# Optimization experiments

Hardware: AMD Instinct MI355X
Metric: run time of the kernel (lower is better)

Reference implementation:

```python
import jax, jax.numpy as jnp
import numpy as np

N = 50000        # nodes
E = 400000       # edges per relation graph
IN_DIM = 64
HID = 128
OUT_DIM = 2
NSEL = 4096
EPS = 0.3        # residual scale
SLOPE = 0.3      # LeakyReLU negative slope


def _leaky(x):
    return jnp.where(x >= 0, x, SLOPE * x)


def _deg_norm(dst):
    # FAGCN-style d = in_degree^{-1/2}; 0 for isolated nodes
    deg = jax.ops.segment_sum(jnp.ones(dst.shape[0], jnp.float32), dst, num_segments=N)
    return jnp.where(deg > 0, jax.lax.rsqrt(jnp.maximum(deg, 1.0)), 0.0)


def _gnn_layer(hf, src, dst, d, gw, gb):
    # gate(concat[h_dst, h_src]) computed as per-node projections then edge gather
    D = hf.shape[1]
    s_dst = hf @ gw[:D]   # [N]
    s_src = hf @ gw[D:]   # [N]
    a = jnp.tanh(s_dst[dst] + s_src[src] + gb)        # [E]
    e = a * d[dst] * d[src]                            # [E]
    msg = hf[src] * e[:, None]                         # [E, D]
    return jax.ops.segment_sum(msg, dst, num_segments=N)


def setup_inputs() -> dict:
    key = jax.random.key(0)
    ks = iter(jax.random.split(key, 48))
    def nrm(shape, scale=0.05):
        return jax.random.normal(next(ks), shape, jnp.float32) * scale
    inp = {}
    inp["h"] = jax.random.normal(next(ks), (N, IN_DIM), jnp.float32)
    for i in (1, 2, 3):
        inp[f"src{i}"] = jax.random.randint(next(ks), (E,), 0, N)
        inp[f"dst{i}"] = jax.random.randint(next(ks), (E,), 0, N)
    inp["nodes"] = jax.random.randint(next(ks), (NSEL,), 0, N)
    inp["t1_w"] = nrm((HID, IN_DIM)); inp["t1_b"] = jnp.zeros((HID,), jnp.float32)
    for i in (1, 2, 3):
        inp[f"gate1_{i}_w"] = nrm((2 * HID,)); inp[f"gate1_{i}_b"] = jnp.zeros((), jnp.float32)
        inp[f"gate2_{i}_w"] = nrm((6 * HID,)); inp[f"gate2_{i}_b"] = jnp.zeros((), jnp.float32)
        inp[f"hw1_{i}"] = nrm((HID, HID))
        inp[f"hw2_{i}"] = nrm((3 * HID, HID))
    inp["t2_w"] = nrm((64, 7 * HID + IN_DIM)); inp["t2_b"] = jnp.zeros((64,), jnp.float32)
    inp["t3_w"] = nrm((OUT_DIM, 64)); inp["t3_b"] = jnp.zeros((OUT_DIM,), jnp.float32)
    return inp


def reference(h, src1, dst1, src2, dst2, src3, dst3, nodes,
              t1_w, t1_b,
              gate1_1_w, gate1_1_b, gate1_2_w, gate1_2_b, gate1_3_w, gate1_3_b,
              gate2_1_w, gate2_1_b, gate2_2_w, gate2_2_b, gate2_3_w, gate2_3_b,
              hw1_1, hw1_2, hw1_3, hw2_1, hw2_2, hw2_3,
              t2_w, t2_b, t3_w, t3_b):
    d1, d2, d3 = _deg_norm(dst1), _deg_norm(dst2), _deg_norm(dst3)
    raw0 = h
    raw1 = _leaky(h @ t1_w.T + t1_b)   # [N, HID] (dropout=identity in eval)
    h1_1 = _leaky((EPS * raw1 + _gnn_layer(raw1, src1, dst1, d1, gate1_1_w, gate1_1_b)) @ hw1_1)
    h1_2 = _leaky((EPS * raw1 + _gnn_layer(raw1, src2, dst2, d2, gate1_2_w, gate1_2_b)) @ hw1_2)
    h1_3 = _leaky((EPS * raw1 + _gnn_layer(raw1, src3, dst3, d3, gate1_3_w, gate1_3_b)) @ hw1_3)
    raw2 = jnp.concatenate([h1_1, h1_2, h1_3], axis=1)   # [N, 3*HID]
    h2_1 = _leaky((EPS * raw2 + _gnn_layer(raw2, src1, dst1, d1, gate2_1_w, gate2_1_b)) @ hw2_1)
    h2_2 = _leaky((EPS * raw2 + _gnn_layer(raw2, src2, dst2, d2, gate2_2_w, gate2_2_b)) @ hw2_2)
    h2_3 = _leaky((EPS * raw2 + _gnn_layer(raw2, src3, dst3, d3, gate2_3_w, gate2_3_b)) @ hw2_3)
    hf = jnp.concatenate([h2_1, h2_2, h2_3, raw0, raw1, raw2], axis=1)  # [N, 7*HID+IN_DIM]
    nf = hf[nodes]                                       # [NSEL, 7*HID+IN_DIM]
    s = _leaky(nf @ t2_w.T + t2_b)
    return s @ t3_w.T + t3_b                             # [NSEL, OUT_DIM]
```

## Files before the change

kernel.cpp:

```cpp
#include <hip/hip_runtime.h>
#include <hip/hip_bf16.h>

#define NN 50000
#define NE 400000
#define IND 64
#define HID 128
#define H3 384
#define FDIM 960
#define NSEL 4096
#define EPSF 0.3f
#define SLOPEF 0.3f
#define SCHUNK 2048
#define NCHUNK 25
#define NBK 196
#define BCAP 4096
#define EPB 4096
#define NOEDGE 0xFFFFFFFFu

typedef __attribute__((ext_vector_type(8))) short bfrag;
typedef __attribute__((ext_vector_type(4))) float f4;
typedef __attribute__((ext_vector_type(8))) unsigned short us8;

__device__ __forceinline__ float leaky1(float v){ return v>=0.f? v : SLOPEF*v; }
__device__ __forceinline__ float b2f(unsigned short u){
  return __uint_as_float(((unsigned)u)<<16);
}
__device__ __forceinline__ unsigned short f2b(float v){
  __hip_bfloat16 b = __float2bfloat16(v);
  return *(unsigned short*)&b;
}

__global__ __launch_bounds__(256) void k_bfill4(
    const int* __restrict__ s0,const int* __restrict__ d0,
    const int* __restrict__ s1,const int* __restrict__ d1,
    const int* __restrict__ s2,const int* __restrict__ d2,
    int* __restrict__ bcnt, unsigned int* __restrict__ pairbuf)
{
  __shared__ unsigned int lbuf[EPB];
  __shared__ int hist[256];
  __shared__ int lbase[256];
  __shared__ int lcur[256];
  __shared__ int gbase[NBK];
  __shared__ int wsum[4];
  const int r = blockIdx.y;
  const int* S = (r==0)?s0:((r==1)?s1:s2);
  const int* D = (r==0)?d0:((r==1)?d1:d2);
  const int e0 = blockIdx.x*EPB;
  const int t = threadIdx.x;
  hist[t] = 0; lcur[t] = 0;
  __syncthreads();

  unsigned int pv[16];
  #pragma unroll
  for (int j=0;j<4;j++){
    int e = e0 + (j*256 + t)*4;
    if (e < NE){
      int4 sv = *(const int4*)&S[e];
      int4 dv = *(const int4*)&D[e];
      pv[j*4+0] = ((unsigned)dv.x<<16)|(unsigned)sv.x;
      pv[j*4+1] = ((unsigned)dv.y<<16)|(unsigned)sv.y;
      pv[j*4+2] = ((unsigned)dv.z<<16)|(unsigned)sv.z;
      pv[j*4+3] = ((unsigned)dv.w<<16)|(unsigned)sv.w;
    } else {
      pv[j*4+0]=NOEDGE; pv[j*4+1]=NOEDGE; pv[j*4+2]=NOEDGE; pv[j*4+3]=NOEDGE;
    }
  }
  #pragma unroll
  for (int i=0;i<16;i++){
    if (pv[i] != NOEDGE){
      atomicAdd(&hist[pv[i]>>24], 1);
    }
  }
  __syncthreads();
  {
    int hv = hist[t];
    int lane = t & 63, wid = t >> 6;
    int x = hv;
    #pragma unroll
    for (int d=1; d<64; d<<=1){ int y=__shfl_up(x,(unsigned)d); if(lane>=d) x+=y; }
    if (lane==63) wsum[wid]=x;
    __syncthreads();
    int wpre = 0;
    if (wid>0) wpre += wsum[0];
    if (wid>1) wpre += wsum[1];
    if (wid>2) wpre += wsum[2];
    lbase[t] = wpre + x - hv;
    if (t < NBK){
      int hh = hist[t];
      gbase[t] = (hh>0) ? atomicAdd(&bcnt[r*NBK+t], hh) : 0;
    }
  }
  __syncthreads();
  #pragma unroll
  for (int i=0;i<16;i++){
    if (pv[i] != NOEDGE){
      int b = (int)(pv[i] >> 24);
      int pos = lbase[b] + atomicAdd(&lcur[b], 1);
      lbuf[pos] = pv[i];
    }
  }
  __syncthreads();
  int tot = min(NE - e0, EPB);
  for (int idx = t; idx < tot; idx += 256){
    unsigned int v = lbuf[idx];
    int b = (int)(v >> 24);
    pairbuf[((size_t)(r*NBK + b))*BCAP + gbase[b] + (idx - lbase[b])] = v;
  }
}

__global__ __launch_bounds__(256) void k_count(const unsigned int* __restrict__ pairbuf,
                                               const int* __restrict__ bcnt,
                                               int* __restrict__ deg){
  __shared__ int hist[256];
  int r = blockIdx.y, b = blockIdx.x;
  int nb0 = b << 8;
  int t = threadIdx.x;
  hist[t] = 0;
  __syncthreads();
  int cnt = bcnt[r*NBK + b];
  const unsigned int* pb = pairbuf + ((size_t)(r*NBK + b))*BCAP;
  for (int e = t; e < cnt; e += 256){
    atomicAdd(&hist[(int)(pb[e] >> 16) - nb0], 1);
  }
  __syncthreads();
  int nidx = nb0 + t;
  if (nidx < NN) deg[r*NN + nidx] = hist[t];
}

__global__ __launch_bounds__(256) void k_scan_a(const int* __restrict__ deg,
    int* __restrict__ off, int* __restrict__ bsum, float* __restrict__ dnv){
  int b = blockIdx.x;
  int r = b / NCHUNK, c = b - r*NCHUNK;
  const int* dg = deg + r*NN;
  int* o = off + r*(NN+1);
  int t = threadIdx.x;
  int base = c*SCHUNK + t*8;
  int v[8];
  #pragma unroll
  for (int j=0;j<8;j++){
    int i = base+j;
    int g = (i<NN)? dg[i] : 0;
    v[j] = g;
    if (i<NN) dnv[r*NN+i] = (g>0)? rsqrtf((float)g) : 0.f;
  }
  int s=0;
  #pragma unroll
  for (int j=0;j<8;j++){ s += v[j]; v[j] = s; }
  int lane = t & 63, wid = t >> 6;
  int x = s;
  #pragma unroll
  for (int d=1; d<64; d<<=1){ int y=__shfl_up(x,(unsigned)d); if(lane>=d) x+=y; }
  __shared__ int ws[4];
  if (lane==63) ws[wid]=x;
  __syncthreads();
  int wpre = 0;
  if (wid>0) wpre += ws[0];
  if (wid>1) wpre += ws[1];
  if (wid>2) wpre += ws[2];
  int excl = wpre + x - s;
  #pragma unroll
  for (int j=0;j<8;j++){ int i=base+j; if (i<NN) o[i+1] = excl + v[j]; }
  if (t==255) bsum[b] = wpre + x;
}

__global__ void k_scan_b(int* __restrict__ bsum){
  int r = threadIdx.x;
  if (r < 3){
    int run = 0;
    for (int c=0;c<NCHUNK;c++){
      int t = bsum[r*NCHUNK+c];
      bsum[r*NCHUNK+c] = run;
      run += t;
    }
  }
}

__global__ __launch_bounds__(256) void k_scan_c(int* __restrict__ off,
                                                const int* __restrict__ bsum){
  int b = blockIdx.x;
  int r = b / NCHUNK, c = b - r*NCHUNK;
  int add = bsum[b];
  int* o = off + r*(NN+1);
  if (threadIdx.x==0 && c==0) o[0]=0;
  int base = c*SCHUNK;
  for (int j=threadIdx.x; j<SCHUNK; j+=256){
    int i = base+j;
    if (i<NN) o[i+1] += add;
  }
}

__global__ __launch_bounds__(256) void k_bsort3(const unsigned int* __restrict__ pairbuf,
                                                const int* __restrict__ bcnt,
                                                const int* __restrict__ off,
                                                unsigned short* __restrict__ csrc){
  __shared__ unsigned short lout[BCAP];
  __shared__ int cur2[256];
  __shared__ int nbase[256];
  int r = blockIdx.y, b = blockIdx.x;
  int nb0 = b << 8;
  const int* offr = off + r*(NN+1);
  int t = threadIdx.x;
  cur2[t] = 0;
  int e0g = offr[nb0];
  int nidx = nb0 + t;
  nbase[t] = (nidx < NN) ? (offr[nidx] - e0g) : 0;
  __syncthreads();
  int cnt = bcnt[r*NBK + b];
  const unsigned int* pb = pairbuf + ((size_t)(r*NBK + b))*BCAP;
  for (int e = t; e < cnt; e += 256){
    unsigned int pv = pb[e];
    int p = (int)(pv >> 16) - nb0;
    int slot = atomicAdd(&cur2[p], 1);
    lout[nbase[p] + slot] = (unsigned short)(pv & 0xffffu);
  }
  __syncthreads();
  unsigned short* op = csrc + (size_t)r*NE + e0g;
  for (int idx = t; idx < cnt; idx += 256) op[idx] = lout[idx];
}

__global__ void k_wprep2(const float* __restrict__ t1w,
    const float* __restrict__ hw1_0, const float* __restrict__ hw1_1, const float* __restrict__ hw1_2,
    const float* __restrict__ hw2_0, const float* __restrict__ hw2_1, const float* __restrict__ hw2_2,
    const float* __restrict__ t2w, const float* __restrict__ h,
    unsigned short* __restrict__ wt1, unsigned short* __restrict__ w1t,
    unsigned short* __restrict__ w2t, unsigned short* __restrict__ wt2,
    unsigned short* __restrict__ hb){
  int t = blockIdx.x*256 + threadIdx.x;
  if (t < 8192){
    wt1[t] = f2b(t1w[t]);
  } else if (t < 57344){
    int e = t - 8192;
    int r = e / 16384, q = e - r*16384;
    int n = q >> 7, k = q & 127;
    const float* W = (r==0)?hw1_0:((r==1)?hw1_1:hw1_2);
    w1t[e] = f2b(W[k*HID + n]);
  } else if (t < 204800){
    int e = t - 57344;
    int r = e / 49152, q = e - r*49152;
    int n = q / H3, k = q - n*H3;
    const float* W = (r==0)?hw2_0:((r==1)?hw2_1:hw2_2);
    w2t[e] = f2b(W[k*HID + n]);
  } else if (t < 266240){
    int e = t - 204800;
    wt2[e] = f2b(t2w[e]);
  } else if (t < 666240){
    int q = t - 266240;
    const float4 a = ((const float4*)h)[q*2];
    const float4 b = ((const float4*)h)[q*2+1];
    us8 o;
    o[0]=f2b(a.x); o[1]=f2b(a.y); o[2]=f2b(a.z); o[3]=f2b(a.w);
    o[4]=f2b(b.x); o[5]=f2b(b.y); o[6]=f2b(b.z); o[7]=f2b(b.w);
    *(us8*)&hb[q*8] = o;
  }
}

__global__ __launch_bounds__(256) void k_mfma_t1(
    const unsigned short* __restrict__ Ab, const unsigned short* __restrict__ W,
    const float* __restrict__ bias, unsigned short* __restrict__ Cb)
{
  __shared__ short As[64][72];
  __shared__ short Bs[128][72];
  const int tid = threadIdx.x;
  const int bm = blockIdx.x*64;

  for (int q = tid; q < 64*8; q += 256){
    int row = q >> 3, c8 = q & 7;
    int grow = bm + row; grow = (grow < NN) ? grow : (NN-1);
    *(us8*)&As[row][c8*8] = *(const us8*)&Ab[(size_t)grow*IND + c8*8];
  }
  for (int q = tid; q < 128*8; q += 256){
    int n = q >> 3, c8 = q & 7;
    *(us8*)&Bs[n][c8*8] = *(const us8*)&W[n*IND + c8*8];
  }
  __syncthreads();

  const int wid = tid >> 6, lane = tid & 63;
  const int wrow = (wid & 1)*32, wcol = (wid >> 1)*64;
  const int fr = lane & 15, fq = lane >> 4;
  f4 acc[2][4];
  #pragma unroll
  for (int mi=0;mi<2;mi++)
    #pragma unroll
    for (int ni=0;ni<4;ni++) acc[mi][ni] = (f4){0.f,0.f,0.f,0.f};

  #pragma unroll
  for (int ks=0; ks<2; ks++){
    int kb = ks*32 + fq*8;
    bfrag a[2], b[4];
    #pragma unroll
    for (int mi=0;mi<2;mi++) a[mi] = *(const bfrag*)&As[wrow + mi*16 + fr][kb];
    #pragma unroll
    for (int ni=0;ni<4;ni++) b[ni] = *(const bfrag*)&Bs[wcol + ni*16 + fr][kb];
    #pragma unroll
    for (int mi=0;mi<2;mi++)
      #pragma unroll
      for (int ni=0;ni<4;ni++)
        acc[mi][ni] = __builtin_amdgcn_mfma_f32_16x16x32_bf16(a[mi], b[ni], acc[mi][ni], 0, 0, 0);
  }

  #pragma unroll
  for (int mi=0;mi<2;mi++){
    int row0 = bm + wrow + mi*16 + fq*4;
    #pragma unroll
    for (int j=0;j<4;j++){
      int row = row0 + j;
      if (row < NN){
        #pragma unroll
        for (int ni=0;ni<4;ni++){
          int col = wcol + ni*16 + fr;
          Cb[(size_t)row*HID + col] = f2b(leaky1(acc[mi][ni][j] + bias[col]));
        }
      }
    }
  }
}

__global__ __launch_bounds__(256) void k_mfma128(
    const unsigned short* __restrict__ Abf, const unsigned short* __restrict__ Wt,
    unsigned short* __restrict__ Cb, int M)
{
  __shared__ short As[64][136];
  __shared__ short Bs[128][136];
  const int r = blockIdx.y;
  const unsigned short* Ar = Abf + (size_t)r*M*HID;
  const unsigned short* W  = Wt + (size_t)r*HID*HID;
  const int tid = threadIdx.x;
  const int bm = blockIdx.x*64;

  for (int q = tid; q < 64*16; q += 256){
    int row = q >> 4, c8 = q & 15;
    int grow = bm + row; grow = (grow < M) ? grow : (M-1);
    *(us8*)&As[row][c8*8] = *(const us8*)&Ar[(size_t)grow*HID + c8*8];
  }
  for (int q = tid; q < 128*16; q += 256){
    int n = q >> 4, c8 = q & 15;
    *(us8*)&Bs[n][c8*8] = *(const us8*)&W[n*HID + c8*8];
  }
  __syncthreads();

  const int wid = tid >> 6, lane = tid & 63;
  const int wrow = (wid & 1)*32, wcol = (wid >> 1)*64;
  const int fr = lane & 15, fq = lane >> 4;
  f4 acc[2][4];
  #pragma unroll
  for (int mi=0;mi<2;mi++)
    #pragma unroll
    for (int ni=0;ni<4;ni++) acc[mi][ni] = (f4){0.f,0.f,0.f,0.f};

  #pragma unroll
  for (int ks=0; ks<4; ks++){
    int kb = ks*32 + fq*8;
    bfrag a[2], b[4];
    #pragma unroll
    for (int mi=0;mi<2;mi++) a[mi] = *(const bfrag*)&As[wrow + mi*16 + fr][kb];
    #pragma unroll
    for (int ni=0;ni<4;ni++) b[ni] = *(const bfrag*)&Bs[wcol + ni*16 + fr][kb];
    #pragma unroll
    for (int mi=0;mi<2;mi++)
      #pragma unroll
      for (int ni=0;ni<4;ni++)
        acc[mi][ni] = __builtin_amdgcn_mfma_f32_16x16x32_bf16(a[mi], b[ni], acc[mi][ni], 0, 0, 0);
  }

  const int coff = r*HID;
  #pragma unroll
  for (int mi=0;mi<2;mi++){
    int row0 = bm + wrow + mi*16 + fq*4;
    #pragma unroll
    for (int j=0;j<4;j++){
      int row = row0 + j;
      if (row < M){
        #pragma unroll
        for (int ni=0;ni<4;ni++){
          Cb[(size_t)row*H3 + coff + wcol + ni*16 + fr] = f2b(leaky1(acc[mi][ni][j]));
        }
      }
    }
  }
}

__global__ __launch_bounds__(256) void k_mfma384(
    const unsigned short* __restrict__ Abf, const unsigned short* __restrict__ Wt,
    unsigned short* __restrict__ nfb)
{
  __shared__ short As[32][72];
  __shared__ short Bs[128][72];
  const int r = blockIdx.y;
  const unsigned short* Ar = Abf + (size_t)r*NSEL*H3;
  const unsigned short* W  = Wt + (size_t)r*HID*H3;
  const int tid = threadIdx.x;
  const int bm = blockIdx.x*32;
  const int wid = tid >> 6, lane = tid & 63;
  const int fr = lane & 15, fq = lane >> 4;
  f4 acc[2][2];
  #pragma unroll
  for (int mi=0;mi<2;mi++)
    #pragma unroll
    for (int ni=0;ni<2;ni++) acc[mi][ni] = (f4){0.f,0.f,0.f,0.f};

  for (int kc=0; kc<6; kc++){
    for (int q = tid; q < 32*8; q += 256){
      int row = q >> 3, c8 = q & 7;
      *(us8*)&As[row][c8*8] = *(const us8*)&Ar[(size_t)(bm+row)*H3 + kc*64 + c8*8];
    }
    for (int q = tid; q < 128*8; q += 256){
      int n = q >> 3, c8 = q & 7;
      *(us8*)&Bs[n][c8*8] = *(const us8*)&W[(size_t)n*H3 + kc*64 + c8*8];
    }
    __syncthreads();
    #pragma unroll
    for (int ks=0; ks<2; ks++){
      int kb = ks*32 + fq*8;
      bfrag a[2], b[2];
      #pragma unroll
      for (int mi=0;mi<2;mi++) a[mi] = *(const bfrag*)&As[mi*16 + fr][kb];
      #pragma unroll
      for (int ni=0;ni<2;ni++) b[ni] = *(const bfrag*)&Bs[wid*32 + ni*16 + fr][kb];
      #pragma unroll
      for (int mi=0;mi<2;mi++)
        #pragma unroll
        for (int ni=0;ni<2;ni++)
          acc[mi][ni] = __builtin_amdgcn_mfma_f32_16x16x32_bf16(a[mi], b[ni], acc[mi][ni], 0, 0, 0);
    }
    __syncthreads();
  }

  #pragma unroll
  for (int mi=0;mi<2;mi++){
    int row0 = bm + mi*16 + fq*4;
    #pragma unroll
    for (int j=0;j<4;j++){
      int i = row0 + j;
      #pragma unroll
      for (int ni=0;ni<2;ni++){
        int col = wid*32 + ni*16 + fr;
        nfb[(size_t)i*FDIM + r*HID + col] = f2b(leaky1(acc[mi][ni][j]));
      }
    }
  }
}

__global__ __launch_bounds__(256) void k_mfma_t2(
    const unsigned short* __restrict__ Abf, const unsigned short* __restrict__ W,
    float* __restrict__ sbuf)
{
  __shared__ short As[32][72];
  __shared__ short Bs[64][72];
  const int tid = threadIdx.x;
  const int bm = blockIdx.x*32;
  const int wid = tid >> 6, lane = tid & 63;
  const int fr = lane & 15, fq = lane >> 4;
  f4 acc[2];
  acc[0] = (f4){0.f,0.f,0.f,0.f};
  acc[1] = (f4){0.f,0.f,0.f,0.f};

  for (int kc=0; kc<15; kc++){
    for (int q = tid; q < 32*8; q += 256){
      int row = q >> 3, c8 = q & 7;
      *(us8*)&As[row][c8*8] = *(const us8*)&Abf[(size_t)(bm+row)*FDIM + kc*64 + c8*8];
    }
    for (int q = tid; q < 64*8; q += 256){
      int n = q >> 3, c8 = q & 7;
      *(us8*)&Bs[n][c8*8] = *(const us8*)&W[(size_t)n*FDIM + kc*64 + c8*8];
    }
    __syncthreads();
    #pragma unroll
    for (int ks=0; ks<2; ks++){
      int kb = ks*32 + fq*8;
      bfrag a[2], b;
      a[0] = *(const bfrag*)&As[fr][kb];
      a[1] = *(const bfrag*)&As[16 + fr][kb];
      b = *(const bfrag*)&Bs[wid*16 + fr][kb];
      acc[0] = __builtin_amdgcn_mfma_f32_16x16x32_bf16(a[0], b, acc[0], 0, 0, 0);
      acc[1] = __builtin_amdgcn_mfma_f32_16x16x32_bf16(a[1], b, acc[1], 0, 0, 0);
    }
    __syncthreads();
  }

  #pragma unroll
  for (int mi=0;mi<2;mi++){
    int row0 = bm + mi*16 + fq*4;
    #pragma unroll
    for (int j=0;j<4;j++){
      sbuf[(size_t)(row0+j)*64 + wid*16 + fr] = acc[mi][j];
    }
  }
}

__global__ __launch_bounds__(256) void k_final_wave(
    const float* __restrict__ sbuf, const float* __restrict__ t2b,
    const float* __restrict__ t3w, const float* __restrict__ t3b,
    float* __restrict__ outp)
{
  int w = (blockIdx.x*256 + threadIdx.x) >> 6;
  int j = threadIdx.x & 63;
  if (w >= NSEL) return;
  float v = leaky1(sbuf[(size_t)w*64 + j] + t2b[j]);
  float a0 = v*t3w[j], a1 = v*t3w[64+j];
  #pragma unroll
  for (int sft=32;sft>0;sft>>=1){
    a0 += __shfl_down(a0,(unsigned)sft);
    a1 += __shfl_down(a1,(unsigned)sft);
  }
  if (j==0){
    outp[2*w+0] = a0 + t3b[0];
    outp[2*w+1] = a1 + t3b[1];
  }
}

template<int D>
__global__ __launch_bounds__(256) void k_scores_g(const unsigned short* __restrict__ X,
    const float* __restrict__ g0, const float* __restrict__ g1, const float* __restrict__ g2,
    float* __restrict__ sd, float* __restrict__ ss){
  const int tid = threadIdx.x;
  const int p = tid & 15;
  const int n = blockIdx.x*16 + (tid >> 4);
  const unsigned short* x = X + (size_t)n*D;
  float a0=0,a1=0,a2=0,a3=0,a4=0,a5=0;
  #pragma unroll
  for (int it=0; it<D/128; it++){
    int k = it*128 + p*8;
    us8 u = *(const us8*)&x[k];
    #pragma unroll
    for (int e=0;e<8;e++){
      float v = b2f(u[e]);
      a0 = fmaf(v, g0[k+e],   a0);  a1 = fmaf(v, g0[D+k+e], a1);
      a2 = fmaf(v, g1[k+e],   a2);  a3 = fmaf(v, g1[D+k+e], a3);
      a4 = fmaf(v, g2[k+e],   a4);  a5 = fmaf(v, g2[D+k+e], a5);
    }
  }
  #pragma unroll
  for (int s=8;s>0;s>>=1){
    a0 += __shfl_xor(a0,(unsigned)s); a1 += __shfl_xor(a1,(unsigned)s);
    a2 += __shfl_xor(a2,(unsigned)s); a3 += __shfl_xor(a3,(unsigned)s);
    a4 += __shfl_xor(a4,(unsigned)s); a5 += __shfl_xor(a5,(unsigned)s);
  }
  if (p==0){
    sd[0*NN+n]=a0; ss[0*NN+n]=a1;
    sd[1*NN+n]=a2; ss[1*NN+n]=a3;
    sd[2*NN+n]=a4; ss[2*NN+n]=a5;
  }
}

__global__ __launch_bounds__(256) void k_gather_f3z(
    const unsigned short* __restrict__ Xb,
    const int* __restrict__ off, const unsigned short* __restrict__ csrc,
    const float* __restrict__ sd, const float* __restrict__ ss,
    const float* __restrict__ dnv,
    const float* __restrict__ gb0, const float* __restrict__ gb1, const float* __restrict__ gb2,
    unsigned short* __restrict__ outp){
  const int tid = threadIdx.x;
  const int lane = tid & 63;
  const int wg = lane >> 4;
  const int p  = lane & 15;
  const int n = blockIdx.x*16 + (tid >> 4);
  us8 rv = *(const us8*)&Xb[(size_t)n*HID + p*8];
  float resid[8];
  #pragma unroll
  for (int i=0;i<8;i++) resid[i] = EPSF * b2f(rv[i]);

  for (int r=0;r<3;r++){
    const int* offr = off + r*(NN+1);
    const unsigned short* csr = csrc + (size_t)r*NE;
    const float* ssr = ss + r*NN;
    const float* dnr = dnv + r*NN;
    float gbv = ((r==0)?gb0:((r==1)?gb1:gb2))[0];
    float sd_n = sd[r*NN + n], dn_n = dnr[n];
    float acc[8];
    #pragma unroll
    for (int i=0;i<8;i++) acc[i] = resid[i];
    int p0 = offr[n], p1 = offr[n+1];
    for (int pc=p0; pc<p1; pc+=16){
      int m = min(16, p1-pc);
      int s = 0; float c = 0.f;
      if (p < m){
        s = csr[pc+p];
        c = tanhf(sd_n + ssr[s] + gbv) * dn_n * dnr[s];
      }
      for (int j=0;j<m;j++){
        int   sj = __shfl(s, wg*16+j);
        float cj = __shfl(c, wg*16+j);
        us8 v = *(const us8*)&Xb[(size_t)sj*HID + p*8];
        #pragma unroll
        for (int i=0;i<8;i++) acc[i] = fmaf(cj, b2f(v[i]), acc[i]);
      }
    }
    us8 o;
    #pragma unroll
    for (int i=0;i<8;i++) o[i] = f2b(acc[i]);
    *(us8*)&outp[((size_t)r*NN + n)*HID + p*8] = o;
  }
}

__global__ __launch_bounds__(256) void k_gather_sel3w2(const unsigned short* __restrict__ Xb,
    const int* __restrict__ nodes,
    const int* __restrict__ off, const unsigned short* __restrict__ csrc,
    const float* __restrict__ sd, const float* __restrict__ ss,
    const float* __restrict__ dnv,
    const float* __restrict__ gb0, const float* __restrict__ gb1, const float* __restrict__ gb2,
    unsigned short* __restrict__ outp){
  const int tid = threadIdx.x;
  const int lane = tid & 63;
  const int wg = lane >> 4;
  const int p  = lane & 15;
  const int i = blockIdx.x*16 + (tid >> 4);
  const int r = blockIdx.y;
  const int n = nodes[i];
  const int* offr = off + r*(NN+1);
  const unsigned short* csr = csrc + (size_t)r*NE;
  const float* ssr = ss + r*NN;
  const float* dnr = dnv + r*NN;
  float gbv = ((r==0)?gb0:((r==1)?gb1:gb2))[0];
  float sd_n = sd[r*NN + n], dn_n = dnr[n];
  float acc[3][8];
  #pragma unroll
  for (int cc=0;cc<3;cc++)
    #pragma unroll
    for (int q=0;q<8;q++) acc[cc][q]=0.f;
  int p0 = offr[n], p1 = offr[n+1];
  for (int pc=p0; pc<p1; pc+=16){
    int m = min(16, p1-pc);
    int s = 0; float c = 0.f;
    if (p < m){
      s = csr[pc+p];
      c = tanhf(sd_n + ssr[s] + gbv) * dn_n * dnr[s];
    }
    for (int j=0;j<m;j++){
      int   sj = __shfl(s, wg*16+j);
      float cj = __shfl(c, wg*16+j);
      const unsigned short* row = &Xb[(size_t)sj*H3];
      #pragma unroll
      for (int cc=0;cc<3;cc++){
        us8 v = *(const us8*)&row[cc*HID + p*8];
        #pragma unroll
        for (int q=0;q<8;q++) acc[cc][q] = fmaf(cj, b2f(v[q]), acc[cc][q]);
      }
    }
  }
  const unsigned short* xrow = &Xb[(size_t)n*H3];
  unsigned short* orow = &outp[((size_t)r*NSEL + i)*H3];
  #pragma unroll
  for (int cc=0;cc<3;cc++){
    us8 v = *(const us8*)&xrow[cc*HID + p*8];
    us8 o;
    #pragma unroll
    for (int q=0;q<8;q++) o[q] = f2b(fmaf(EPSF, b2f(v[q]), acc[cc][q]));
    *(us8*)&orow[cc*HID + p*8] = o;
  }
}

__global__ __launch_bounds__(256) void k_nf_fillb(const unsigned short* __restrict__ hb,
    const unsigned short* __restrict__ raw1b, const unsigned short* __restrict__ raw2b,
    const int* __restrict__ nodes, unsigned short* __restrict__ nfb){
  int t = blockIdx.x*256 + threadIdx.x;
  if (t >= NSEL*72) return;
  int i = t/72, c = t - i*72;
  int n = nodes[i];
  us8 v; int col;
  if (c < 8)       { v = *(const us8*)&hb[(size_t)n*IND + c*8];           col = 384 + c*8; }
  else if (c < 24) { int q=c-8;  v = *(const us8*)&raw1b[(size_t)n*HID + q*8]; col = 448 + q*8; }
  else             { int q=c-24; v = *(const us8*)&raw2b[(size_t)n*H3  + q*8]; col = 576 + q*8; }
  *(us8*)&nfb[(size_t)i*FDIM + col] = v;
}

extern "C" void kernel_launch(void* const* d_in, const int* in_sizes, int n_in,
                              void* d_out, int out_size, void* d_ws, size_t ws_size,
                              hipStream_t stream){
  if (n_in < 32) return;
  const float* h = (const float*)d_in[0];
  const int* src[3] = {(const int*)d_in[1], (const int*)d_in[3], (const int*)d_in[5]};
  const int* dst[3] = {(const int*)d_in[2], (const int*)d_in[4], (const int*)d_in[6]};
  const int* nodes = (const int*)d_in[7];
  const float* t1w = (const float*)d_in[8];
  const float* t1b = (const float*)d_in[9];

  bool dictOrder = (in_sizes[12] == 768);
  const float *g1w[3],*g1b[3],*g2w[3],*g2b[3],*hw1[3],*hw2[3];
  for (int r=0;r<3;r++){
    if (dictOrder){
      int base = 10 + r*6;
      g1w[r]=(const float*)d_in[base+0]; g1b[r]=(const float*)d_in[base+1];
      g2w[r]=(const float*)d_in[base+2]; g2b[r]=(const float*)d_in[base+3];
      hw1[r]=(const float*)d_in[base+4]; hw2[r]=(const float*)d_in[base+5];
    } else {
      g1w[r]=(const float*)d_in[10+2*r]; g1b[r]=(const float*)d_in[11+2*r];
      g2w[r]=(const float*)d_in[16+2*r]; g2b[r]=(const float*)d_in[17+2*r];
      hw1[r]=(const float*)d_in[22+r];   hw2[r]=(const float*)d_in[25+r];
    }
  }
  const float* t2w = (const float*)d_in[28];
  const float* t2b = (const float*)d_in[29];
  const float* t3w = (const float*)d_in[30];
  const float* t3b = (const float*)d_in[31];
  float* outp = (float*)d_out;

  char* w = (char*)d_ws;
  auto carve = [&](size_t bytes)->void*{
    void* p = (void*)w;
    w += ((bytes + 255) & ~size_t(255));
    return p;
  };
  int*   deg  = (int*)  carve((size_t)(3*NN+1024)*4);
  int*   bcnt = deg + 3*NN;
  int*   off  = (int*)  carve((size_t)3*(NN+1)*4);
  float* dnv  = (float*)carve((size_t)3*NN*4);
  int*   bsum = (int*)  carve((size_t)128*4);
  unsigned short* csrc = (unsigned short*)carve((size_t)3*NE*2);
  float* sd1  = (float*)carve((size_t)3*NN*4);
  float* ss1  = (float*)carve((size_t)3*NN*4);
  float* sd2  = (float*)carve((size_t)3*NN*4);
  float* ss2  = (float*)carve((size_t)3*NN*4);
  unsigned short* wt1 = (unsigned short*)carve((size_t)HID*IND*2);
  unsigned short* w1t = (unsigned short*)carve((size_t)3*HID*HID*2);
  unsigned short* w2t = (unsigned short*)carve((size_t)3*HID*H3*2);
  unsigned short* wt2 = (unsigned short*)carve((size_t)64*FDIM*2);
  unsigned short* hb  = (unsigned short*)carve((size_t)NN*IND*2);
  unsigned short* raw1b = (unsigned short*)carve((size_t)NN*HID*2);
  unsigned short* raw2b = (unsigned short*)carve((size_t)NN*H3*2);
  size_t ubytes = (size_t)3*NN*HID*2;
  float* ureg = (float*)carve(ubytes);
  unsigned int* pairbuf = (unsigned int*)ureg;
  unsigned short* pre1b = (unsigned short*)ureg;
  unsigned short* pre2b = (unsigned short*)ureg;
  float* sbuf = (float*)((char*)ureg + (size_t)16*1024*1024);
  unsigned short* nfb = (unsigned short*)carve((size_t)NSEL*FDIM*2);

  hipMemsetAsync(bcnt, 0, (size_t)1024*4, stream);
  k_bfill4<<<dim3((NE+EPB-1)/EPB, 3), 256, 0, stream>>>(
      src[0],dst[0],src[1],dst[1],src[2],dst[2], bcnt, pairbuf);
  k_count <<<dim3(NBK,3), 256, 0, stream>>>(pairbuf, bcnt, deg);
  k_scan_a<<<3*NCHUNK, 256, 0, stream>>>(deg, off, bsum, dnv);
  k_scan_b<<<1, 64, 0, stream>>>(bsum);
  k_scan_c<<<3*NCHUNK, 256, 0, stream>>>(off, bsum);
  k_bsort3<<<dim3(NBK,3), 256, 0, stream>>>(pairbuf, bcnt, off, csrc);

  k_wprep2<<<(666240+255)/256, 256, 0, stream>>>(
      t1w, hw1[0], hw1[1], hw1[2], hw2[0], hw2[1], hw2[2], t2w, h,
      wt1, w1t, w2t, wt2, hb);

  k_mfma_t1<<<(NN+63)/64, 256, 0, stream>>>(hb, wt1, t1b, raw1b);

  k_scores_g<HID><<<NN/16, 256, 0, stream>>>(raw1b, g1w[0], g1w[1], g1w[2], sd1, ss1);

  k_gather_f3z<<<NN/16, 256, 0, stream>>>(raw1b, off, csrc,
      sd1, ss1, dnv, g1b[0], g1b[1], g1b[2], pre1b);
  k_mfma128<<<dim3((NN+63)/64, 3), 256, 0, stream>>>(pre1b, w1t, raw2b, NN);

  k_scores_g<H3><<<NN/16, 256, 0, stream>>>(raw2b, g2w[0], g2w[1], g2w[2], sd2, ss2);

  k_gather_sel3w2<<<dim3(NSEL/16, 3), 256, 0, stream>>>(raw2b, nodes, off, csrc,
      sd2, ss2, dnv, g2b[0], g2b[1], g2b[2], pre2b);

  k_mfma384<<<dim3(NSEL/32, 3), 256, 0, stream>>>(pre2b, w2t, nfb);

  k_nf_fillb<<<(NSEL*72+255)/256, 256, 0, stream>>>(hb, raw1b, raw2b, nodes, nfb);

  k_mfma_t2<<<NSEL/32, 256, 0, stream>>>(nfb, wt2, sbuf);
  k_final_wave<<<(NSEL*64+255)/256, 256, 0, stream>>>(sbuf, t2b, t3w, t3b, outp);
}
```

Baseline: 207.3 us.

## Fuse CSR count/scan/sort into one bucket kernel and prefetch gather rows

Replaces the count, three-stage scan and bucket-sort kernels with a single kernel per bucket. Each block derives its global edge offset by reducing the preceding bucket counts, builds a local histogram and scan, and writes offsets, degree norms and sorted sources in one pass. This removes four launches and the degree array round-trip. The gather kernels also load row offsets up front and software-pipeline the neighbour row loads one edge ahead, hiding load latency at the cost of extra registers.

```diff
diff --git a/kernel.cpp b/kernel.cpp
--- a/kernel.cpp
+++ b/kernel.cpp
@@ -10,8 +10,6 @@
 #define NSEL 4096
 #define EPSF 0.3f
 #define SLOPEF 0.3f
-#define SCHUNK 2048
-#define NCHUNK 25
 #define NBK 196
 #define BCAP 4096
 #define EPB 4096
@@ -67,9 +65,7 @@
   }
   #pragma unroll
   for (int i=0;i<16;i++){
-    if (pv[i] != NOEDGE){
-      atomicAdd(&hist[pv[i]>>24], 1);
-    }
+    if (pv[i] != NOEDGE) atomicAdd(&hist[pv[i]>>24], 1);
   }
   __syncthreads();
   {
@@ -108,113 +104,72 @@
   }
 }
 
-__global__ __launch_bounds__(256) void k_count(const unsigned int* __restrict__ pairbuf,
-                                               const int* __restrict__ bcnt,
-                                               int* __restrict__ deg){
+__global__ __launch_bounds__(256) void k_bsort4(
+    const unsigned int* __restrict__ pairbuf,
+    const int* __restrict__ bcnt,
+    int* __restrict__ off, float* __restrict__ dnv,
+    unsigned short* __restrict__ csrc)
+{
+  __shared__ unsigned short lout[BCAP];
   __shared__ int hist[256];
-  int r = blockIdx.y, b = blockIdx.x;
-  int nb0 = b << 8;
-  int t = threadIdx.x;
-  hist[t] = 0;
-  __syncthreads();
-  int cnt = bcnt[r*NBK + b];
+  __shared__ int excl[256];
+  __shared__ int cur[256];
+  __shared__ int red[256];
+  __shared__ int wsum[4];
+  const int r = blockIdx.y, b = blockIdx.x;
+  const int nb0 = b << 8;
+  const int t = threadIdx.x;
+  red[t] = (t < b) ? bcnt[r*NBK + t] : 0;
+  hist[t] = 0; cur[t] = 0;
+  __syncthreads();
+  #pragma unroll
+  for (int sdv=128; sdv>0; sdv>>=1){
+    if (t < sdv) red[t] += red[t+sdv];
+    __syncthreads();
+  }
+  const int bbase = red[0];
+  const int cnt = bcnt[r*NBK + b];
   const unsigned int* pb = pairbuf + ((size_t)(r*NBK + b))*BCAP;
-  for (int e = t; e < cnt; e += 256){
-    atomicAdd(&hist[(int)(pb[e] >> 16) - nb0], 1);
+  unsigned int pv[16];
+  #pragma unroll
+  for (int j=0;j<16;j++){
+    int e = j*256 + t;
+    pv[j] = (e < cnt) ? pb[e] : NOEDGE;
+    if (pv[j] != NOEDGE) atomicAdd(&hist[(int)(pv[j]>>16) - nb0], 1);
+  }
+  __syncthreads();
+  {
+    int hv = hist[t];
+    int lane = t & 63, wid = t >> 6;
+    int x = hv;
+    #pragma unroll
+    for (int d=1; d<64; d<<=1){ int y=__shfl_up(x,(unsigned)d); if(lane>=d) x+=y; }
+    if (lane==63) wsum[wid]=x;
+    __syncthreads();
+    int wpre = 0;
+    if (wid>0) wpre += wsum[0];
+    if (wid>1) wpre += wsum[1];
+    if (wid>2) wpre += wsum[2];
+    excl[t] = wpre + x - hv;
   }
   __syncthreads();
   int nidx = nb0 + t;
-  if (nidx < NN) deg[r*NN + nidx] = hist[t];
-}
-
-__global__ __launch_bounds__(256) void k_scan_a(const int* __restrict__ deg,
-    int* __restrict__ off, int* __restrict__ bsum, float* __restrict__ dnv){
-  int b = blockIdx.x;
-  int r = b / NCHUNK, c = b - r*NCHUNK;
-  const int* dg = deg + r*NN;
-  int* o = off + r*(NN+1);
-  int t = threadIdx.x;
-  int base = c*SCHUNK + t*8;
-  int v[8];
-  #pragma unroll
-  for (int j=0;j<8;j++){
-    int i = base+j;
-    int g = (i<NN)? dg[i] : 0;
-    v[j] = g;
-    if (i<NN) dnv[r*NN+i] = (g>0)? rsqrtf((float)g) : 0.f;
-  }
-  int s=0;
-  #pragma unroll
-  for (int j=0;j<8;j++){ s += v[j]; v[j] = s; }
-  int lane = t & 63, wid = t >> 6;
-  int x = s;
-  #pragma unroll
-  for (int d=1; d<64; d<<=1){ int y=__shfl_up(x,(unsigned)d); if(lane>=d) x+=y; }
-  __shared__ int ws[4];
-  if (lane==63) ws[wid]=x;
-  __syncthreads();
-  int wpre = 0;
-  if (wid>0) wpre += ws[0];
-  if (wid>1) wpre += ws[1];
-  if (wid>2) wpre += ws[2];
-  int excl = wpre + x - s;
-  #pragma unroll
-  for (int j=0;j<8;j++){ int i=base+j; if (i<NN) o[i+1] = excl + v[j]; }
-  if (t==255) bsum[b] = wpre + x;
-}
-
-__global__ void k_scan_b(int* __restrict__ bsum){
-  int r = threadIdx.x;
-  if (r < 3){
-    int run = 0;
-    for (int c=0;c<NCHUNK;c++){
-      int t = bsum[r*NCHUNK+c];
-      bsum[r*NCHUNK+c] = run;
-      run += t;
-    }
-  }
-}
-
-__global__ __launch_bounds__(256) void k_scan_c(int* __restrict__ off,
-                                                const int* __restrict__ bsum){
-  int b = blockIdx.x;
-  int r = b / NCHUNK, c = b - r*NCHUNK;
-  int add = bsum[b];
-  int* o = off + r*(NN+1);
-  if (threadIdx.x==0 && c==0) o[0]=0;
-  int base = c*SCHUNK;
-  for (int j=threadIdx.x; j<SCHUNK; j+=256){
-    int i = base+j;
-    if (i<NN) o[i+1] += add;
-  }
-}
-
-__global__ __launch_bounds__(256) void k_bsort3(const unsigned int* __restrict__ pairbuf,
-                                                const int* __restrict__ bcnt,
-                                                const int* __restrict__ off,
-                                                unsigned short* __restrict__ csrc){
-  __shared__ unsigned short lout[BCAP];
-  __shared__ int cur2[256];
-  __shared__ int nbase[256];
-  int r = blockIdx.y, b = blockIdx.x;
-  int nb0 = b << 8;
-  const int* offr = off + r*(NN+1);
-  int t = threadIdx.x;
-  cur2[t] = 0;
-  int e0g = offr[nb0];
-  int nidx = nb0 + t;
-  nbase[t] = (nidx < NN) ? (offr[nidx] - e0g) : 0;
-  __syncthreads();
-  int cnt = bcnt[r*NBK + b];
-  const unsigned int* pb = pairbuf + ((size_t)(r*NBK + b))*BCAP;
-  for (int e = t; e < cnt; e += 256){
-    unsigned int pv = pb[e];
-    int p = (int)(pv >> 16) - nb0;
-    int slot = atomicAdd(&cur2[p], 1);
-    lout[nbase[p] + slot] = (unsigned short)(pv & 0xffffu);
-  }
-  __syncthreads();
-  unsigned short* op = csrc + (size_t)r*NE + e0g;
+  if (nidx < NN){
+    off[r*(NN+1) + nidx] = bbase + excl[t];
+    int g = hist[t];
+    dnv[r*NN + nidx] = (g>0) ? rsqrtf((float)g) : 0.f;
+  }
+  if (b == NBK-1 && t == 0) off[r*(NN+1) + NN] = bbase + cnt;
+  #pragma unroll
+  for (int j=0;j<16;j++){
+    if (pv[j] != NOEDGE){
+      int pn = (int)(pv[j] >> 16) - nb0;
+      int slot = atomicAdd(&cur[pn], 1);
+      lout[excl[pn] + slot] = (unsigned short)(pv[j] & 0xffffu);
+    }
+  }
+  __syncthreads();
+  unsigned short* op = csrc + (size_t)r*NE + bbase;
   for (int idx = t; idx < cnt; idx += 256) op[idx] = lout[idx];
 }
 
@@ -555,12 +510,17 @@
   const int p  = lane & 15;
   const int n = blockIdx.x*16 + (tid >> 4);
   us8 rv = *(const us8*)&Xb[(size_t)n*HID + p*8];
+  int p0a[3], p1a[3];
+  #pragma unroll
+  for (int r=0;r<3;r++){
+    p0a[r] = off[r*(NN+1) + n];
+    p1a[r] = off[r*(NN+1) + n + 1];
+  }
   float resid[8];
   #pragma unroll
   for (int i=0;i<8;i++) resid[i] = EPSF * b2f(rv[i]);
 
   for (int r=0;r<3;r++){
-    const int* offr = off + r*(NN+1);
     const unsigned short* csr = csrc + (size_t)r*NE;
     const float* ssr = ss + r*NN;
     const float* dnr = dnv + r*NN;
@@ -569,7 +529,7 @@
     float acc[8];
     #pragma unroll
     for (int i=0;i<8;i++) acc[i] = resid[i];
-    int p0 = offr[n], p1 = offr[n+1];
+    int p0 = p0a[r], p1 = p1a[r];
     for (int pc=p0; pc<p1; pc+=16){
       int m = min(16, p1-pc);
       int s = 0; float c = 0.f;
@@ -577,12 +537,19 @@
         s = csr[pc+p];
         c = tanhf(sd_n + ssr[s] + gbv) * dn_n * dnr[s];
       }
-      for (int j=0;j<m;j++){
-        int   sj = __shfl(s, wg*16+j);
-        float cj = __shfl(c, wg*16+j);
-        us8 v = *(const us8*)&Xb[(size_t)sj*HID + p*8];
+      int   sj = __shfl(s, wg*16);
+      float cj = __shfl(c, wg*16);
+      us8 v = *(const us8*)&Xb[(size_t)sj*HID + p*8];
+      for (int j=1;j<=m;j++){
+        us8 vn; float cn = 0.f;
+        if (j < m){
+          int sn = __shfl(s, wg*16+j);
+          cn = __shfl(c, wg*16+j);
+          vn = *(const us8*)&Xb[(size_t)sn*HID + p*8];
+        }
         #pragma unroll
         for (int i=0;i<8;i++) acc[i] = fmaf(cj, b2f(v[i]), acc[i]);
+        v = vn; cj = cn;
       }
     }
     us8 o;
@@ -625,16 +592,29 @@
       s = csr[pc+p];
       c = tanhf(sd_n + ssr[s] + gbv) * dn_n * dnr[s];
     }
-    for (int j=0;j<m;j++){
-      int   sj = __shfl(s, wg*16+j);
-      float cj = __shfl(c, wg*16+j);
-      const unsigned short* row = &Xb[(size_t)sj*H3];
+    int   sj = __shfl(s, wg*16);
+    float cj = __shfl(c, wg*16);
+    const unsigned short* row = &Xb[(size_t)sj*H3];
+    us8 v0 = *(const us8*)&row[0*HID + p*8];
+    us8 v1 = *(const us8*)&row[1*HID + p*8];
+    us8 v2 = *(const us8*)&row[2*HID + p*8];
+    for (int j=1;j<=m;j++){
+      us8 n0, n1, n2; float cn = 0.f;
+      if (j < m){
+        int sn = __shfl(s, wg*16+j);
+        cn = __shfl(c, wg*16+j);
+        const unsigned short* rw = &Xb[(size_t)sn*H3];
+        n0 = *(const us8*)&rw[0*HID + p*8];
+        n1 = *(const us8*)&rw[1*HID + p*8];
+        n2 = *(const us8*)&rw[2*HID + p*8];
+      }
       #pragma unroll
-      for (int cc=0;cc<3;cc++){
-        us8 v = *(const us8*)&row[cc*HID + p*8];
-        #pragma unroll
-        for (int q=0;q<8;q++) acc[cc][q] = fmaf(cj, b2f(v[q]), acc[cc][q]);
+      for (int q=0;q<8;q++){
+        acc[0][q] = fmaf(cj, b2f(v0[q]), acc[0][q]);
+        acc[1][q] = fmaf(cj, b2f(v1[q]), acc[1][q]);
+        acc[2][q] = fmaf(cj, b2f(v2[q]), acc[2][q]);
       }
+      v0 = n0; v1 = n1; v2 = n2; cj = cn;
     }
   }
   const unsigned short* xrow = &Xb[(size_t)n*H3];
@@ -700,11 +680,9 @@
     w += ((bytes + 255) & ~size_t(255));
     return p;
   };
-  int*   deg  = (int*)  carve((size_t)(3*NN+1024)*4);
-  int*   bcnt = deg + 3*NN;
+  int*   bcnt = (int*)  carve((size_t)1024*4);
   int*   off  = (int*)  carve((size_t)3*(NN+1)*4);
   float* dnv  = (float*)carve((size_t)3*NN*4);
-  int*   bsum = (int*)  carve((size_t)128*4);
   unsigned short* csrc = (unsigned short*)carve((size_t)3*NE*2);
   float* sd1  = (float*)carve((size_t)3*NN*4);
   float* ss1  = (float*)carve((size_t)3*NN*4);
@@ -728,11 +706,7 @@
   hipMemsetAsync(bcnt, 0, (size_t)1024*4, stream);
   k_bfill4<<<dim3((NE+EPB-1)/EPB, 3), 256, 0, stream>>>(
       src[0],dst[0],src[1],dst[1],src[2],dst[2], bcnt, pairbuf);
-  k_count <<<dim3(NBK,3), 256, 0, stream>>>(pairbuf, bcnt, deg);
-  k_scan_a<<<3*NCHUNK, 256, 0, stream>>>(deg, off, bsum, dnv);
-  k_scan_b<<<1, 64, 0, stream>>>(bsum);
-  k_scan_c<<<3*NCHUNK, 256, 0, stream>>>(off, bsum);
-  k_bsort3<<<dim3(NBK,3), 256, 0, stream>>>(pairbuf, bcnt, off, csrc);
+  k_bsort4<<<dim3(NBK,3), 256, 0, stream>>>(pairbuf, bcnt, off, dnv, csrc);
 
   k_wprep2<<<(666240+255)/256, 256, 0, stream>>>(
       t1w, hw1[0], hw1[1], hw1[2], hw2[0], hw2[1], hw2[2], t2w, h,
```

New measurement: 197.0 us. 4.9% less time.
